# Performance work log

Measured on AMD Instinct MI355X. Metric: run time of the kernel, lower is better.

## Reference

```python
import jax, jax.numpy as jnp
import numpy as np
from jax import lax

C = 256

def conv1x1(x, w, b):
    # x: [B,C,H,W], w: [O,C], b: [O]
    return jnp.einsum('bchw,oc->bohw', x, w) + b[None, :, None, None]

def conv3x3_s2(x, w, b):
    # x: [B,C,H,W], w: [O,C,3,3] -> stride 2, pad 1
    y = lax.conv_general_dilated(x, w, window_strides=(2, 2),
                                 padding=((1, 1), (1, 1)),
                                 dimension_numbers=('NCHW', 'OIHW', 'NCHW'))
    return y + b[None, :, None, None]

def to_qv(x):
    # [B,C,H,W] -> permute(0,2,3,1) -> view [B,H,W,1,C]
    return jnp.transpose(x, (0, 2, 3, 1))[:, :, :, None, :]

def to_k(x):
    # [B,C,H,W] -> permute(0,2,3,1) -> view [B,H,W,C,1]
    return jnp.transpose(x, (0, 2, 3, 1))[:, :, :, :, None]

def upsample2x_nearest(x):
    return jnp.repeat(jnp.repeat(x, 2, axis=2), 2, axis=3)


def setup_inputs() -> dict:
    key = jax.random.key(0)
    ks = jax.random.split(key, 20)
    x1 = jax.random.normal(ks[0], (2, C, 128, 128), dtype=jnp.float32)
    x2 = jax.random.normal(ks[1], (2, C, 64, 64), dtype=jnp.float32)
    s = 0.05
    d = {'x1': x1, 'x2': x2}
    names = ['q1', 'q2', 'ks1', 'ks2', 'kup', 'v1', 'v2']
    for i, n in enumerate(names):
        d[n + '_w'] = jax.random.normal(ks[2 + 2 * i], (C, C), dtype=jnp.float32) * s
        d[n + '_b'] = jax.random.normal(ks[3 + 2 * i], (C,), dtype=jnp.float32) * s
    d['kdown_w'] = jax.random.normal(ks[16], (C, C, 3, 3), dtype=jnp.float32) * s
    d['kdown_b'] = jax.random.normal(ks[17], (C,), dtype=jnp.float32) * s
    return d


def reference(x1, x2, q1_w, q1_b, q2_w, q2_b, ks1_w, ks1_b, ks2_w, ks2_b,
              kup_w, kup_b, v1_w, v1_b, v2_w, v2_b, kdown_w, kdown_b):
    q1 = to_qv(conv1x1(x1, q1_w, q1_b))            # [B,128,128,1,C]
    q2 = to_qv(conv1x1(x2, q2_w, q2_b))            # [B,64,64,1,C]
    k_up = to_k(upsample2x_nearest(conv1x1(x2, kup_w, kup_b)))  # [B,128,128,C,1]
    k_self_1 = to_k(conv1x1(x1, ks1_w, ks1_b))     # [B,128,128,C,1]
    k_self_2 = to_k(conv1x1(x2, ks2_w, ks2_b))     # [B,64,64,C,1]
    k_down = to_k(conv3x3_s2(x1, kdown_w, kdown_b))  # [B,64,64,C,1]
    v1 = to_qv(conv1x1(x1, v1_w, v1_b))            # [B,128,128,1,C]
    v2 = to_qv(conv1x1(x2, v2_w, v2_b))            # [B,64,64,1,C]
    return (q1, q2, k_up, k_self_1, k_self_2, k_down, v1, v2)
```

## Files before the change

kernel.cpp:

```cpp
#include <hip/hip_runtime.h>
#include <hip/hip_bf16.h>
#include <stdint.h>


typedef __attribute__((ext_vector_type(8))) __bf16 bf16x8;
typedef __attribute__((ext_vector_type(4))) float f32x4;
typedef __attribute__((ext_vector_type(8))) unsigned short u16x8;

typedef const __attribute__((address_space(1))) uint32_t* gptr_t;
typedef __attribute__((address_space(3))) uint32_t* lptr_t;

__device__ __forceinline__ void cp16(void* lds, const void* g) {
  gptr_t gp = reinterpret_cast<gptr_t>(reinterpret_cast<uintptr_t>(g));
  lptr_t lp = reinterpret_cast<lptr_t>(
      static_cast<uint32_t>(reinterpret_cast<uintptr_t>(lds)));
  __builtin_amdgcn_global_load_lds(gp, lp, 16, 0, 0);
}

__global__ void nchw2nhwc_v2(const float* __restrict__ src,
                             uint16_t* __restrict__ dst,
                             int H, int W, int pad) {
  __shared__ float tile[64][65];
  const int tid = threadIdx.x;
  const int b = blockIdx.z / H;
  const int h = blockIdx.z - b * H;
  const int wt = blockIdx.x * 64;
  const int ct = blockIdx.y * 64;
  const long cs = (long)H * W;
  const float* s = src + ((long)(b * 256 + ct) * H + h) * W + wt;
  const int rw = tid >> 4;
  const int rf = tid & 15;
#pragma unroll
  for (int p = 0; p < 4; p++) {
    const int cl = p * 16 + rw;
    const float4 v = *(const float4*)(s + (long)cl * cs + rf * 4);
    tile[cl][rf * 4 + 0] = v.x;
    tile[cl][rf * 4 + 1] = v.y;
    tile[cl][rf * 4 + 2] = v.z;
    tile[cl][rf * 4 + 3] = v.w;
  }
  __syncthreads();
  const int wl0 = tid >> 3;
  const int cg = tid & 7;
  const int Wp = W + 2 * pad;
  const long rowb = ((long)(b * (H + 2 * pad) + h + pad)) * Wp + pad + wt;
#pragma unroll
  for (int p = 0; p < 2; p++) {
    const int wl = p * 32 + wl0;
    u16x8 u;
#pragma unroll
    for (int k = 0; k < 8; k++) {
      __hip_bfloat16 hb = __float2bfloat16(tile[cg * 8 + k][wl]);
      u[k] = *reinterpret_cast<uint16_t*>(&hb);
    }
    *(u16x8*)(dst + (rowb + wl) * 256 + ct + cg * 8) = u;
  }
}

struct WArgs {
  const float* w1[7];
  const float* kdw;
};

__global__ void convert_weights_v2(WArgs a, uint16_t* __restrict__ wf) {
  const int idx = blockIdx.x * 256 + threadIdx.x;
  const int mat = idx >> 13;
  const int g = idx & 8191;
  const int jg = g >> 9;
  const int kc = (g >> 6) & 7;
  const int lane = g & 63;
  const int o = jg * 16 + (lane & 15);
  const int k0 = kc * 32 + (lane >> 4) * 8;
  float f[8];
  if (mat < 7) {
    const float* w = a.w1[mat];
    const float4 v0 = *(const float4*)(w + o * 256 + k0);
    const float4 v1 = *(const float4*)(w + o * 256 + k0 + 4);
    f[0] = v0.x; f[1] = v0.y; f[2] = v0.z; f[3] = v0.w;
    f[4] = v1.x; f[5] = v1.y; f[6] = v1.z; f[7] = v1.w;
  } else {
    const int tap = mat - 7;
#pragma unroll
    for (int e = 0; e < 8; e++)
      f[e] = a.kdw[(long)o * 2304 + (long)(k0 + e) * 9 + tap];
  }
  u16x8 u;
#pragma unroll
  for (int e = 0; e < 8; e++) {
    __hip_bfloat16 hb = __float2bfloat16(f[e]);
    u[e] = *reinterpret_cast<uint16_t*>(&hb);
  }
  *(u16x8*)(wf + (long)idx * 8) = u;
}

struct Job {
  const uint16_t* A;
  const uint16_t* Wf;
  const float* bias;
  float* out;
  int mtiles;
  int mode;
  int tap0;
};
struct JobArgs {
  Job j[10];
};

__global__ __launch_bounds__(256, 2) void fused_gemm(JobArgs args) {
  const Job jb = args.j[blockIdx.z];
  if ((int)blockIdx.x >= jb.mtiles) return;
  const int mtile = blockIdx.x;
  const int mode = jb.mode;

  __shared__ __align__(16) uint16_t lA[32768];

  const int tid = threadIdx.x;
  const int lane = tid & 63;
  const int wave = tid >> 6;
  const int wr = wave & 1;
  const int wc = wave >> 1;
  const int q = lane >> 4;
  const int l15 = lane & 15;

  const uint16_t* rowA[2];
  {
    const int rbase = wave * 16 + (lane >> 2);
#pragma unroll
    for (int rh = 0; rh < 2; rh++) {
      const int m = mtile * 128 + rh * 64 + rbase;
      long p;
      if (mode == 0) {
        p = ((long)((m >> 14) * 130 + ((m >> 7) & 127) + 1)) * 130 + (m & 127) + 1;
      } else if (mode == 3) {
        p = ((long)((m >> 12) * 130 + 2 * ((m >> 6) & 63))) * 130 + 2 * (m & 63);
      } else {
        p = m;
      }
      rowA[rh] = jb.A + p * 256 + (lane & 3) * 8;
    }
  }

  f32x4 acc[4][8] = {};
  const int ntaps = (mode == 3) ? 3 : 1;

  for (int t = 0; t < ntaps; t++) {
    long aoff = 0;
    const uint16_t* wf = jb.Wf;
    if (mode == 3) {
      const int tap = jb.tap0 + t;
      const int kh = tap / 3;
      const int kw = tap - kh * 3;
      aoff = (long)(kh * 130 + kw) * 256;
      wf = jb.Wf + (long)tap * 65536;
    }
    if (t) __syncthreads();
#pragma unroll
    for (int kap = 0; kap < 16; kap++) {
      const uint16_t* src = rowA[kap & 1] + aoff + (kap >> 1) * 32;
      cp16(lA + (kap * 256 + wave * 64) * 8, src);
    }
    __syncthreads();

#pragma unroll
    for (int kc = 0; kc < 8; kc++) {
      bf16x8 av[4];
#pragma unroll
      for (int i = 0; i < 4; i++)
        av[i] = *(const bf16x8*)(lA + (kc * 128 + wr * 64 + i * 16 + l15) * 32 + q * 8);
#pragma unroll
      for (int j = 0; j < 8; j++) {
        const bf16x8 bv =
            *(const bf16x8*)(wf + ((long)((wc * 8 + j) * 8 + kc) * 64 + lane) * 8);
#pragma unroll
        for (int i = 0; i < 4; i++)
          acc[i][j] = __builtin_amdgcn_mfma_f32_16x16x32_bf16(av[i], bv,
                                                              acc[i][j], 0, 0, 0);
      }
    }
  }

  const int nb = wc * 128 + l15;
  const int mb = mtile * 128 + wr * 64 + q * 4;
  if (mode == 3) {
#pragma unroll
    for (int j = 0; j < 8; j++) {
      const int n = nb + j * 16;
      const float bv = jb.bias ? jb.bias[n] : 0.0f;
#pragma unroll
      for (int i = 0; i < 4; i++) {
        const int m0 = mb + i * 16;
#pragma unroll
        for (int r = 0; r < 4; r++)
          atomicAdd(jb.out + (long)(m0 + r) * 256 + n, acc[i][j][r] + bv);
      }
    }
  } else if (mode == 2) {
#pragma unroll
    for (int j = 0; j < 8; j++) {
      const int n = nb + j * 16;
      const float bv = jb.bias[n];
#pragma unroll
      for (int i = 0; i < 4; i++) {
        const int m0 = mb + i * 16;
#pragma unroll
        for (int r = 0; r < 4; r++) {
          const int m = m0 + r;
          const int b = m >> 12;
          const int h2 = (m >> 6) & 63;
          const int w2 = m & 63;
          const float val = acc[i][j][r] + bv;
          float* o = jb.out + ((long)(b * 128 + 2 * h2) * 128 + 2 * w2) * 256 + n;
          o[0] = val;
          o[256] = val;
          o[32768] = val;
          o[32768 + 256] = val;
        }
      }
    }
  } else {
#pragma unroll
    for (int j = 0; j < 8; j++) {
      const int n = nb + j * 16;
      const float bv = jb.bias[n];
#pragma unroll
      for (int i = 0; i < 4; i++) {
        const int m0 = mb + i * 16;
#pragma unroll
        for (int r = 0; r < 4; r++)
          jb.out[(long)(m0 + r) * 256 + n] = acc[i][j][r] + bv;
      }
    }
  }
}

extern "C" void kernel_launch(void* const* d_in, const int* in_sizes, int n_in,
                              void* d_out, int out_size, void* d_ws,
                              size_t ws_size, hipStream_t stream) {
  (void)in_sizes; (void)n_in; (void)out_size; (void)ws_size;
  const float* x1 = (const float*)d_in[0];
  const float* x2 = (const float*)d_in[1];
  float* out = (float*)d_out;

  uint16_t* x1p = (uint16_t*)d_ws;
  uint16_t* x2b = x1p + 8652800;
  uint16_t* wf = x2b + 2097152;

  hipMemsetAsync(x1p, 0, 8652800 * sizeof(uint16_t), stream);
  hipMemsetAsync(out + 29360128L, 0, 2097152 * sizeof(float), stream);

  nchw2nhwc_v2<<<dim3(2, 4, 256), 256, 0, stream>>>(x1, x1p, 128, 128, 1);
  nchw2nhwc_v2<<<dim3(1, 4, 128), 256, 0, stream>>>(x2, x2b, 64, 64, 0);

  WArgs wa;
  wa.w1[0] = (const float*)d_in[2];
  wa.w1[1] = (const float*)d_in[4];
  wa.w1[2] = (const float*)d_in[6];
  wa.w1[3] = (const float*)d_in[8];
  wa.w1[4] = (const float*)d_in[10];
  wa.w1[5] = (const float*)d_in[12];
  wa.w1[6] = (const float*)d_in[14];
  wa.kdw = (const float*)d_in[16];
  convert_weights_v2<<<512, 256, 0, stream>>>(wa, wf);

  const uint16_t* wfk = wf + 7 * 65536;
  JobArgs ja;
  ja.j[0] = {x1p, wfk, (const float*)d_in[17], out + 29360128L, 64, 3, 0};
  ja.j[1] = {x1p, wfk, nullptr,                out + 29360128L, 64, 3, 3};
  ja.j[2] = {x1p, wfk, nullptr,                out + 29360128L, 64, 3, 6};
  ja.j[3] = {x1p, wf + 0 * 65536, (const float*)d_in[3],  out + 0L,        256, 0, 0};
  ja.j[4] = {x1p, wf + 2 * 65536, (const float*)d_in[7],  out + 18874368L, 256, 0, 0};
  ja.j[5] = {x1p, wf + 5 * 65536, (const float*)d_in[13], out + 31457280L, 256, 0, 0};
  ja.j[6] = {x2b, wf + 4 * 65536, (const float*)d_in[11], out + 10485760L, 64, 2, 0};
  ja.j[7] = {x2b, wf + 1 * 65536, (const float*)d_in[5],  out + 8388608L,  64, 1, 0};
  ja.j[8] = {x2b, wf + 3 * 65536, (const float*)d_in[9],  out + 27262976L, 64, 1, 0};
  ja.j[9] = {x2b, wf + 6 * 65536, (const float*)d_in[15], out + 39845888L, 64, 1, 0};
  fused_gemm<<<dim3(256, 1, 10), 256, 0, stream>>>(ja);
}
```

Baseline: 299.1 us.

## Restructure 3x3 conv as 64x128 tiles with full tap loop, drop memsets and atomics

The strided 3x3 conv no longer splits its nine taps across three jobs that combine through atomicAdd into a zeroed output. Each block now owns a 64x128 output tile and loops over all taps, then writes the result with plain stores. The two memsets are replaced by a kernel that zeroes only the padding border, and that kernel also does the weight conversion. The two transposes are merged into one launch, and the GEMM uses a flat 1D grid with no idle blocks. This removes atomic traffic, full-buffer memsets and several launches, but each conv block is smaller and runs nine serial taps, which could lengthen the tail.

```diff
diff --git a/kernel.cpp b/kernel.cpp
--- a/kernel.cpp
+++ b/kernel.cpp
@@ -17,13 +17,80 @@
   __builtin_amdgcn_global_load_lds(gp, lp, 16, 0, 0);
 }
 
-__global__ void nchw2nhwc_v2(const float* __restrict__ src,
-                             uint16_t* __restrict__ dst,
-                             int H, int W, int pad) {
+struct WArgs {
+  const float* w1[7];
+  const float* kdw;
+};
+
+__global__ void prep(WArgs a, uint16_t* __restrict__ wf,
+                     uint16_t* __restrict__ x1p) {
+  const int bx = blockIdx.x;
+  if (bx < 512) {
+    const int idx = bx * 256 + threadIdx.x;
+    const int mat = idx >> 13;
+    const int g = idx & 8191;
+    const int jg = g >> 9;
+    const int kc = (g >> 6) & 7;
+    const int lane = g & 63;
+    const int o = jg * 16 + (lane & 15);
+    const int k0 = kc * 32 + (lane >> 4) * 8;
+    float f[8];
+    if (mat < 7) {
+      const float* w = a.w1[mat];
+      const float4 v0 = *(const float4*)(w + o * 256 + k0);
+      const float4 v1 = *(const float4*)(w + o * 256 + k0 + 4);
+      f[0] = v0.x; f[1] = v0.y; f[2] = v0.z; f[3] = v0.w;
+      f[4] = v1.x; f[5] = v1.y; f[6] = v1.z; f[7] = v1.w;
+    } else {
+      const int tap = mat - 7;
+#pragma unroll
+      for (int e = 0; e < 8; e++)
+        f[e] = a.kdw[(long)o * 2304 + (long)(k0 + e) * 9 + tap];
+    }
+    u16x8 u;
+#pragma unroll
+    for (int e = 0; e < 8; e++) {
+      __hip_bfloat16 hb = __float2bfloat16(f[e]);
+      u[e] = *reinterpret_cast<uint16_t*>(&hb);
+    }
+    *(u16x8*)(wf + (long)idx * 8) = u;
+  } else {
+    const int c = (bx - 512) * 256 + threadIdx.x;
+    const int b = (c >= 16512) ? 1 : 0;
+    const int cc = c - b * 16512;
+    int h, w, g8;
+    if (cc < 4160) {
+      h = 0; w = cc >> 5; g8 = cc & 31;
+    } else if (cc < 8320) {
+      const int s = cc - 4160; h = 129; w = s >> 5; g8 = s & 31;
+    } else if (cc < 12416) {
+      const int s = cc - 8320; h = 1 + (s >> 5); w = 0; g8 = s & 31;
+    } else {
+      const int s = cc - 12416; h = 1 + (s >> 5); w = 129; g8 = s & 31;
+    }
+    u16x8 z = {};
+    *(u16x8*)(x1p + (((long)(b * 130 + h)) * 130 + w) * 256 + g8 * 8) = z;
+  }
+}
+
+__global__ void transpose_all(const float* __restrict__ x1,
+                              const float* __restrict__ x2,
+                              uint16_t* __restrict__ x1p,
+                              uint16_t* __restrict__ x2b) {
+  const float* src;
+  uint16_t* dst;
+  int H, W, pad, b, h;
+  if ((int)blockIdx.z < 256) {
+    src = x1; dst = x1p; H = 128; W = 128; pad = 1;
+    b = blockIdx.z >> 7; h = blockIdx.z & 127;
+  } else {
+    if (blockIdx.x) return;
+    const int t = blockIdx.z - 256;
+    src = x2; dst = x2b; H = 64; W = 64; pad = 0;
+    b = t >> 6; h = t & 63;
+  }
   __shared__ float tile[64][65];
   const int tid = threadIdx.x;
-  const int b = blockIdx.z / H;
-  const int h = blockIdx.z - b * H;
   const int wt = blockIdx.x * 64;
   const int ct = blockIdx.y * 64;
   const long cs = (long)H * W;
@@ -57,59 +124,25 @@
   }
 }
 
-struct WArgs {
-  const float* w1[7];
-  const float* kdw;
-};
-
-__global__ void convert_weights_v2(WArgs a, uint16_t* __restrict__ wf) {
-  const int idx = blockIdx.x * 256 + threadIdx.x;
-  const int mat = idx >> 13;
-  const int g = idx & 8191;
-  const int jg = g >> 9;
-  const int kc = (g >> 6) & 7;
-  const int lane = g & 63;
-  const int o = jg * 16 + (lane & 15);
-  const int k0 = kc * 32 + (lane >> 4) * 8;
-  float f[8];
-  if (mat < 7) {
-    const float* w = a.w1[mat];
-    const float4 v0 = *(const float4*)(w + o * 256 + k0);
-    const float4 v1 = *(const float4*)(w + o * 256 + k0 + 4);
-    f[0] = v0.x; f[1] = v0.y; f[2] = v0.z; f[3] = v0.w;
-    f[4] = v1.x; f[5] = v1.y; f[6] = v1.z; f[7] = v1.w;
-  } else {
-    const int tap = mat - 7;
-#pragma unroll
-    for (int e = 0; e < 8; e++)
-      f[e] = a.kdw[(long)o * 2304 + (long)(k0 + e) * 9 + tap];
-  }
-  u16x8 u;
-#pragma unroll
-  for (int e = 0; e < 8; e++) {
-    __hip_bfloat16 hb = __float2bfloat16(f[e]);
-    u[e] = *reinterpret_cast<uint16_t*>(&hb);
-  }
-  *(u16x8*)(wf + (long)idx * 8) = u;
-}
-
 struct Job {
   const uint16_t* A;
   const uint16_t* Wf;
   const float* bias;
   float* out;
-  int mtiles;
+  int start;
   int mode;
-  int tap0;
 };
 struct JobArgs {
-  Job j[10];
+  Job j[8];
 };
 
 __global__ __launch_bounds__(256, 2) void fused_gemm(JobArgs args) {
-  const Job jb = args.j[blockIdx.z];
-  if ((int)blockIdx.x >= jb.mtiles) return;
-  const int mtile = blockIdx.x;
+  int jid = 0;
+#pragma unroll
+  for (int t = 1; t < 8; t++)
+    if ((int)blockIdx.x >= args.j[t].start) jid = t;
+  const Job jb = args.j[jid];
+  const int bid = blockIdx.x - jb.start;
   const int mode = jb.mode;
 
   __shared__ __align__(16) uint16_t lA[32768];
@@ -122,6 +155,60 @@
   const int q = lane >> 4;
   const int l15 = lane & 15;
 
+  if (mode == 3) {
+    const int mtile = bid >> 1;
+    const int ntile = bid & 1;
+    const int row = mtile * 64 + wave * 16 + (lane >> 2);
+    const long p =
+        ((long)((row >> 12) * 130 + 2 * ((row >> 6) & 63))) * 130 + 2 * (row & 63);
+    const uint16_t* rowA = jb.A + p * 256 + (lane & 3) * 8;
+
+    f32x4 acc[2][4] = {};
+    for (int tap = 0; tap < 9; tap++) {
+      const int kh = tap / 3;
+      const int kw = tap - kh * 3;
+      const long aoff = (long)(kh * 130 + kw) * 256;
+      const uint16_t* wf = jb.Wf + (long)tap * 65536;
+      if (tap) __syncthreads();
+#pragma unroll
+      for (int kap = 0; kap < 8; kap++)
+        cp16(lA + (kap * 256 + wave * 64) * 8, rowA + aoff + kap * 32);
+      __syncthreads();
+#pragma unroll
+      for (int kc = 0; kc < 8; kc++) {
+        bf16x8 av[2];
+#pragma unroll
+        for (int i = 0; i < 2; i++)
+          av[i] = *(const bf16x8*)(lA + (kc * 64 + wr * 32 + i * 16 + l15) * 32 + q * 8);
+#pragma unroll
+        for (int j = 0; j < 4; j++) {
+          const bf16x8 bv = *(const bf16x8*)(
+              wf + ((long)((ntile * 8 + wc * 4 + j) * 8 + kc) * 64 + lane) * 8);
+#pragma unroll
+          for (int i = 0; i < 2; i++)
+            acc[i][j] = __builtin_amdgcn_mfma_f32_16x16x32_bf16(av[i], bv,
+                                                                acc[i][j], 0, 0, 0);
+        }
+      }
+    }
+    const int nb = ntile * 128 + wc * 64 + l15;
+    const int mb = mtile * 64 + wr * 32 + q * 4;
+#pragma unroll
+    for (int j = 0; j < 4; j++) {
+      const int n = nb + j * 16;
+      const float bvs = jb.bias[n];
+#pragma unroll
+      for (int i = 0; i < 2; i++) {
+        const int m0 = mb + i * 16;
+#pragma unroll
+        for (int r = 0; r < 4; r++)
+          jb.out[(long)(m0 + r) * 256 + n] = acc[i][j][r] + bvs;
+      }
+    }
+    return;
+  }
+
+  const int mtile = bid;
   const uint16_t* rowA[2];
   {
     const int rbase = wave * 16 + (lane >> 2);
@@ -131,8 +218,6 @@
       long p;
       if (mode == 0) {
         p = ((long)((m >> 14) * 130 + ((m >> 7) & 127) + 1)) * 130 + (m & 127) + 1;
-      } else if (mode == 3) {
-        p = ((long)((m >> 12) * 130 + 2 * ((m >> 6) & 63))) * 130 + 2 * (m & 63);
       } else {
         p = m;
       }
@@ -140,65 +225,36 @@
     }
   }
 
+#pragma unroll
+  for (int kap = 0; kap < 16; kap++)
+    cp16(lA + (kap * 256 + wave * 64) * 8, rowA[kap & 1] + (kap >> 1) * 32);
+  __syncthreads();
+
   f32x4 acc[4][8] = {};
-  const int ntaps = (mode == 3) ? 3 : 1;
-
-  for (int t = 0; t < ntaps; t++) {
-    long aoff = 0;
-    const uint16_t* wf = jb.Wf;
-    if (mode == 3) {
-      const int tap = jb.tap0 + t;
-      const int kh = tap / 3;
-      const int kw = tap - kh * 3;
-      aoff = (long)(kh * 130 + kw) * 256;
-      wf = jb.Wf + (long)tap * 65536;
-    }
-    if (t) __syncthreads();
-#pragma unroll
-    for (int kap = 0; kap < 16; kap++) {
-      const uint16_t* src = rowA[kap & 1] + aoff + (kap >> 1) * 32;
-      cp16(lA + (kap * 256 + wave * 64) * 8, src);
-    }
-    __syncthreads();
-
-#pragma unroll
-    for (int kc = 0; kc < 8; kc++) {
-      bf16x8 av[4];
+#pragma unroll
+  for (int kc = 0; kc < 8; kc++) {
+    bf16x8 av[4];
+#pragma unroll
+    for (int i = 0; i < 4; i++)
+      av[i] = *(const bf16x8*)(lA + (kc * 128 + wr * 64 + i * 16 + l15) * 32 + q * 8);
+#pragma unroll
+    for (int j = 0; j < 8; j++) {
+      const bf16x8 bv =
+          *(const bf16x8*)(jb.Wf + ((long)((wc * 8 + j) * 8 + kc) * 64 + lane) * 8);
 #pragma unroll
       for (int i = 0; i < 4; i++)
-        av[i] = *(const bf16x8*)(lA + (kc * 128 + wr * 64 + i * 16 + l15) * 32 + q * 8);
-#pragma unroll
-      for (int j = 0; j < 8; j++) {
-        const bf16x8 bv =
-            *(const bf16x8*)(wf + ((long)((wc * 8 + j) * 8 + kc) * 64 + lane) * 8);
-#pragma unroll
-        for (int i = 0; i < 4; i++)
-          acc[i][j] = __builtin_amdgcn_mfma_f32_16x16x32_bf16(av[i], bv,
-                                                              acc[i][j], 0, 0, 0);
-      }
+        acc[i][j] = __builtin_amdgcn_mfma_f32_16x16x32_bf16(av[i], bv,
+                                                            acc[i][j], 0, 0, 0);
     }
   }
 
   const int nb = wc * 128 + l15;
   const int mb = mtile * 128 + wr * 64 + q * 4;
-  if (mode == 3) {
+  if (mode == 2) {
 #pragma unroll
     for (int j = 0; j < 8; j++) {
       const int n = nb + j * 16;
-      const float bv = jb.bias ? jb.bias[n] : 0.0f;
-#pragma unroll
-      for (int i = 0; i < 4; i++) {
-        const int m0 = mb + i * 16;
-#pragma unroll
-        for (int r = 0; r < 4; r++)
-          atomicAdd(jb.out + (long)(m0 + r) * 256 + n, acc[i][j][r] + bv);
-      }
-    }
-  } else if (mode == 2) {
-#pragma unroll
-    for (int j = 0; j < 8; j++) {
-      const int n = nb + j * 16;
-      const float bv = jb.bias[n];
+      const float bvs = jb.bias[n];
 #pragma unroll
       for (int i = 0; i < 4; i++) {
         const int m0 = mb + i * 16;
@@ -208,8 +264,9 @@
           const int b = m >> 12;
           const int h2 = (m >> 6) & 63;
           const int w2 = m & 63;
-          const float val = acc[i][j][r] + bv;
-          float* o = jb.out + ((long)(b * 128 + 2 * h2) * 128 + 2 * w2) * 256 + n;
+          const float val = acc[i][j][r] + bvs;
+          float* o =
+              jb.out + ((long)(b * 128 + 2 * h2) * 128 + 2 * w2) * 256 + n;
           o[0] = val;
           o[256] = val;
           o[32768] = val;
@@ -221,13 +278,13 @@
 #pragma unroll
     for (int j = 0; j < 8; j++) {
       const int n = nb + j * 16;
-      const float bv = jb.bias[n];
+      const float bvs = jb.bias[n];
 #pragma unroll
       for (int i = 0; i < 4; i++) {
         const int m0 = mb + i * 16;
 #pragma unroll
         for (int r = 0; r < 4; r++)
-          jb.out[(long)(m0 + r) * 256 + n] = acc[i][j][r] + bv;
+          jb.out[(long)(m0 + r) * 256 + n] = acc[i][j][r] + bvs;
       }
     }
   }
@@ -244,12 +301,6 @@
   uint16_t* x1p = (uint16_t*)d_ws;
   uint16_t* x2b = x1p + 8652800;
   uint16_t* wf = x2b + 2097152;
-
-  hipMemsetAsync(x1p, 0, 8652800 * sizeof(uint16_t), stream);
-  hipMemsetAsync(out + 29360128L, 0, 2097152 * sizeof(float), stream);
-
-  nchw2nhwc_v2<<<dim3(2, 4, 256), 256, 0, stream>>>(x1, x1p, 128, 128, 1);
-  nchw2nhwc_v2<<<dim3(1, 4, 128), 256, 0, stream>>>(x2, x2b, 64, 64, 0);
 
   WArgs wa;
   wa.w1[0] = (const float*)d_in[2];
@@ -260,19 +311,17 @@
   wa.w1[5] = (const float*)d_in[12];
   wa.w1[6] = (const float*)d_in[14];
   wa.kdw = (const float*)d_in[16];
-  convert_weights_v2<<<512, 256, 0, stream>>>(wa, wf);
-
-  const uint16_t* wfk = wf + 7 * 65536;
+  prep<<<641, 256, 0, stream>>>(wa, wf, x1p);
+  transpose_all<<<dim3(2, 4, 384), 256, 0, stream>>>(x1, x2, x1p, x2b);
+
   JobArgs ja;
-  ja.j[0] = {x1p, wfk, (const float*)d_in[17], out + 29360128L, 64, 3, 0};
-  ja.j[1] = {x1p, wfk, nullptr,                out + 29360128L, 64, 3, 3};
-  ja.j[2] = {x1p, wfk, nullptr,                out + 29360128L, 64, 3, 6};
-  ja.j[3] = {x1p, wf + 0 * 65536, (const float*)d_in[3],  out + 0L,        256, 0, 0};
-  ja.j[4] = {x1p, wf + 2 * 65536, (const float*)d_in[7],  out + 18874368L, 256, 0, 0};
-  ja.j[5] = {x1p, wf + 5 * 65536, (const float*)d_in[13], out + 31457280L, 256, 0, 0};
-  ja.j[6] = {x2b, wf + 4 * 65536, (const float*)d_in[11], out + 10485760L, 64, 2, 0};
-  ja.j[7] = {x2b, wf + 1 * 65536, (const float*)d_in[5],  out + 8388608L,  64, 1, 0};
-  ja.j[8] = {x2b, wf + 3 * 65536, (const float*)d_in[9],  out + 27262976L, 64, 1, 0};
-  ja.j[9] = {x2b, wf + 6 * 65536, (const float*)d_in[15], out + 39845888L, 64, 1, 0};
-  fused_gemm<<<dim3(256, 1, 10), 256, 0, stream>>>(ja);
-}
+  ja.j[0] = {x1p, wf + 7 * 65536, (const float*)d_in[17], out + 29360128L, 0,    3};
+  ja.j[1] = {x1p, wf + 0 * 65536, (const float*)d_in[3],  out + 0L,        256,  0};
+  ja.j[2] = {x1p, wf + 2 * 65536, (const float*)d_in[7],  out + 18874368L, 512,  0};
+  ja.j[3] = {x1p, wf + 5 * 65536, (const float*)d_in[13], out + 31457280L, 768,  0};
+  ja.j[4] = {x2b, wf + 4 * 65536, (const float*)d_in[11], out + 10485760L, 1024, 2};
+  ja.j[5] = {x2b, wf + 1 * 65536, (const float*)d_in[5],  out + 8388608L,  1088, 1};
+  ja.j[6] = {x2b, wf + 3 * 65536, (const float*)d_in[9],  out + 27262976L, 1152, 1};
+  ja.j[7] = {x2b, wf + 6 * 65536, (const float*)d_in[15], out + 39845888L, 1216, 1};
+  fused_gemm<<<1280, 256, 0, stream>>>(ja);
+}
```

Measured after the change: 286.4 us. -4.2%, faster.
